# Performance work log

Measured on AMD Instinct MI355X. Metric: run time of the kernel, lower is better.

## Reference

```python
import jax, jax.numpy as jnp
import numpy as np

BS = 32  # block size
EPS = 1e-5

def _bn(h, g, b):
    # training-mode batchnorm over (N,H,W) of the gathered block batch
    mu = h.mean((0, 2, 3), keepdims=True)
    var = h.var((0, 2, 3), keepdims=True)
    return (h - mu) * jax.lax.rsqrt(var + EPS) * g.reshape(1, -1, 1, 1) + b.reshape(1, -1, 1, 1)

def setup_inputs() -> dict:
    key = jax.random.key(0)
    ks = jax.random.split(key, 12)
    B, Cin, H, W, Cout = 4, 128, 256, 256, 256
    Hb, Wb = H // BS, W // BS
    x = jax.random.normal(ks[0], (B, Cin, H, W), dtype=jnp.float32)
    rng = np.random.default_rng(0)
    flat = np.sort(rng.choice(B * Hb * Wb, size=128, replace=False)).astype(np.int32)
    bi = flat // (Hb * Wb)
    by = (flat % (Hb * Wb)) // Wb
    bx = flat % Wb
    block_idx = jnp.asarray(np.stack([bi, by, bx], axis=1), dtype=jnp.int32)  # [Nact,3]
    s1 = 1.0 / np.sqrt(Cin)
    s2 = 1.0 / np.sqrt(Cout * 9)
    return {
        "x": x,
        "w1": jax.random.normal(ks[1], (Cout, Cin), jnp.float32) * s1,
        "b1": jnp.zeros((Cout,), jnp.float32),
        "g1": jnp.ones((Cout,), jnp.float32),
        "be1": jnp.zeros((Cout,), jnp.float32),
        "w2": jax.random.normal(ks[2], (Cout, Cout, 3, 3), jnp.float32) * s2,
        "b2": jnp.zeros((Cout,), jnp.float32),
        "g2": jnp.ones((Cout,), jnp.float32),
        "be2": jnp.zeros((Cout,), jnp.float32),
        "wd": jax.random.normal(ks[3], (Cout, Cin), jnp.float32) * s1,
        "bd": jnp.zeros((Cout,), jnp.float32),
        "block_idx": block_idx,
    }

def reference(x, w1, b1, g1, be1, w2, b2, g2, be2, wd, bd, block_idx):
    B, Cin, H, W = x.shape
    Cout = w1.shape[0]
    Hb, Wb = H // BS, W // BS
    # --- sparse gather: [Nact, Cin, BS, BS] ---
    xb = x.reshape(B, Cin, Hb, BS, Wb, BS).transpose(0, 2, 4, 1, 3, 5)
    xb = xb.reshape(B * Hb * Wb, Cin, BS, BS)
    flat = block_idx[:, 0] * (Hb * Wb) + block_idx[:, 1] * Wb + block_idx[:, 2]
    dense = xb[flat]
    # --- dense conv stack on active blocks ---
    h = jnp.einsum('nchw,oc->nohw', dense, w1) + b1.reshape(1, -1, 1, 1)
    h = jax.nn.relu(_bn(h, g1, be1))  # relu is inplace in torch -> feeds conv2
    h = jax.lax.conv_general_dilated(h, w2, (1, 1), 'SAME',
                                     dimension_numbers=('NCHW', 'OIHW', 'NCHW'))
    h = h + b2.reshape(1, -1, 1, 1)
    dense_y = jax.nn.relu(_bn(h, g2, be2))
    # NOTE: original conv3/bn3 output is dead code (scatter uses dense_y); omitted.
    # --- dense base path (in_channels != out_channels -> downsample 1x1 conv) ---
    ybase = jnp.einsum('nchw,oc->nohw', x, wd) + bd.reshape(1, -1, 1, 1)
    # --- sparse scatter (overwrite, add=False) ---
    yb = ybase.reshape(B, Cout, Hb, BS, Wb, BS).transpose(0, 2, 4, 1, 3, 5)
    yb = yb.reshape(B * Hb * Wb, Cout, BS, BS)
    yb = yb.at[flat].set(dense_y)
    y = yb.reshape(B, Hb, Wb, Cout, BS, BS).transpose(0, 3, 1, 4, 2, 5)
    return y.reshape(B, Cout, H, W)
```

## Files before the change

kernel.cpp:

```cpp
#include <hip/hip_runtime.h>
#include <stdint.h>

#define CIN  128
#define COUT 256
#define HH   256
#define WW   256
#define BSZ  32
#define HB   8
#define WB   8
#define NBLK 256
#define P2   34
#define PIX2 1156

typedef __attribute__((ext_vector_type(8))) short bfx8;
typedef __attribute__((ext_vector_type(4))) float f32x4;

#define MFMA(a,b,c) __builtin_amdgcn_mfma_f32_16x16x32_bf16((a),(b),(c),0,0,0)

typedef const __attribute__((address_space(1))) unsigned int gu32;
typedef __attribute__((address_space(3))) unsigned int lu32;
#define GLOAD16(g, p) __builtin_amdgcn_global_load_lds((gu32*)(g), (lu32*)(p), 16, 0, 0)

static __device__ __forceinline__ float bf2f(unsigned short u){
  union { unsigned int i; float f; } v; v.i = ((unsigned int)u)<<16; return v.f;
}
static __device__ __forceinline__ unsigned short f2bf(float f){
  union { float f; unsigned int i; } v; v.f = f;
  unsigned int r = v.i + 0x7fffu + ((v.i>>16)&1u);
  return (unsigned short)(r>>16);
}

__global__ void k_prep(const float* __restrict__ w1, const float* __restrict__ wd,
                       const float* __restrict__ w2,
                       unsigned short* __restrict__ w1b, unsigned short* __restrict__ wdb,
                       unsigned short* __restrict__ w2t){
  int i = blockIdx.x*256 + threadIdx.x;
  if (i < COUT*CIN){ w1b[i] = f2bf(w1[i]); wdb[i] = f2bf(wd[i]); }
  if (i < COUT*COUT*9){
    int co = i/2304, r = i - co*2304;
    int ci = r/9,   tp = r - ci*9;
    w2t[((size_t)tp*COUT + co)*COUT + ci] = f2bf(w2[i]);
  }
}

__global__ void k_lists(const int* __restrict__ bidx, int nact,
                        int* __restrict__ flags, int* __restrict__ inact){
  int t = threadIdx.x;
  if (t < nact){
    int f = bidx[t*3]*(HB*WB) + bidx[t*3+1]*WB + bidx[t*3+2];
    flags[f] = 1;
  }
  __syncthreads();
  if (t == 0){
    int c = 0;
    for (int f = 0; f < NBLK; ++f) if (!flags[f]) inact[c++] = f;
  }
}

template<int MODE>
__global__ __launch_bounds__(256) void k_gemm1(
    const float* __restrict__ x, const unsigned short* __restrict__ wgt,
    const int* __restrict__ bidx, const int* __restrict__ inact,
    const float* __restrict__ bd, unsigned short* __restrict__ h1p,
    float* __restrict__ out, float* __restrict__ part){
  __shared__ unsigned short lds[2*5120];
  int rg = blockIdx.x, cot = blockIdx.y, z = blockIdx.z;
  int bi, by, bx;
  if (MODE == 0){ bi = bidx[z*3]; by = bidx[z*3+1]; bx = bidx[z*3+2]; }
  else { int fl = inact[z]; bi = fl>>6; by = (fl>>3)&7; bx = fl&7; }
  int t = threadIdx.x, l = t&63, wid = t>>6;
  int wc = wid>>1, wp = wid&1;
  int y0 = rg*4;
  int co_w = cot*128 + wc*64;

  const unsigned short* wb = wgt + (size_t)(co_w + (l&15))*CIN + ((l>>4)*8);
  bfx8 wfrag[4][4];
  #pragma unroll
  for (int kc = 0; kc < 4; ++kc)
    #pragma unroll
    for (int m = 0; m < 4; ++m)
      wfrag[kc][m] = *(const bfx8*)(wb + kc*32 + (size_t)m*16*CIN);

  const float* xb = x + (size_t)bi*CIN*HH*WW + (size_t)(by*BSZ + y0)*WW + bx*BSZ;
  float4 ra[2], rb_[2];
  auto ldreg = [&](int kc){
    #pragma unroll
    for (int j = 0; j < 2; ++j){
      int u = j*256 + t;
      int ci0 = (u>>5)*2 + kc*32;
      int p = (u&31)*4;
      const float* s = xb + (size_t)ci0*(HH*WW) + (p>>5)*WW + (p&31);
      ra[j]  = *(const float4*)s;
      rb_[j] = *(const float4*)(s + HH*WW);
    }
  };
  auto wrlds = [&](int buf){
    #pragma unroll
    for (int j = 0; j < 2; ++j){
      int u = j*256 + t;
      int ci0 = (u>>5)*2;
      int p = (u&31)*4;
      unsigned short* d = &lds[buf*5120 + ci0];
      *(ushort2*)&d[(p+0)*40] = make_ushort2(f2bf(ra[j].x), f2bf(rb_[j].x));
      *(ushort2*)&d[(p+1)*40] = make_ushort2(f2bf(ra[j].y), f2bf(rb_[j].y));
      *(ushort2*)&d[(p+2)*40] = make_ushort2(f2bf(ra[j].z), f2bf(rb_[j].z));
      *(ushort2*)&d[(p+3)*40] = make_ushort2(f2bf(ra[j].w), f2bf(rb_[j].w));
    }
  };

  f32x4 acc[4][4] = {};
  ldreg(0);
  for (int kc = 0; kc < 4; ++kc){
    wrlds(kc&1);
    if (kc < 3) ldreg(kc+1);
    __syncthreads();
    const unsigned short* lb = &lds[(kc&1)*5120];
    #pragma unroll
    for (int f = 0; f < 4; ++f){
      bfx8 b = *(const bfx8*)&lb[(wp*64 + f*16 + (l&15))*40 + (l>>4)*8];
      acc[0][f] = MFMA(wfrag[kc][0], b, acc[0][f]);
      acc[1][f] = MFMA(wfrag[kc][1], b, acc[1][f]);
      acc[2][f] = MFMA(wfrag[kc][2], b, acc[2][f]);
      acc[3][f] = MFMA(wfrag[kc][3], b, acc[3][f]);
    }
  }

  #pragma unroll
  for (int m = 0; m < 4; ++m){
    int co = co_w + m*16 + ((l>>4)<<2);
    #pragma unroll
    for (int f = 0; f < 4; ++f){
      int px = wp*64 + f*16 + (l&15);
      int ly = px>>5, lx = px&31;
      if (MODE == 0){
        *(ushort4*)&h1p[((size_t)z*PIX2 + (size_t)(y0+ly+1)*P2 + (lx+1))*COUT + co] =
          make_ushort4(f2bf(acc[m][f][0]), f2bf(acc[m][f][1]),
                       f2bf(acc[m][f][2]), f2bf(acc[m][f][3]));
      } else {
        int gy = by*BSZ + y0 + ly, gx = bx*BSZ + lx;
        #pragma unroll
        for (int j = 0; j < 4; ++j)
          out[(((size_t)bi*COUT + co + j)*HH + gy)*WW + gx] = acc[m][f][j] + bd[co+j];
      }
    }
  }

  if (MODE == 0){
    float s_[4][4], q_[4][4];
    #pragma unroll
    for (int m = 0; m < 4; ++m)
      #pragma unroll
      for (int j = 0; j < 4; ++j){
        float s = 0.f, q = 0.f;
        #pragma unroll
        for (int f = 0; f < 4; ++f){ float v = acc[m][f][j]; s += v; q += v*v; }
        s_[m][j] = s; q_[m][j] = q;
      }
    #pragma unroll
    for (int off = 1; off < 16; off <<= 1)
      #pragma unroll
      for (int m = 0; m < 4; ++m)
        #pragma unroll
        for (int j = 0; j < 4; ++j){
          s_[m][j] += __shfl_xor(s_[m][j], off);
          q_[m][j] += __shfl_xor(q_[m][j], off);
        }
    if ((l&15) == 0){
      int grp = z & 15;
      #pragma unroll
      for (int m = 0; m < 4; ++m)
        #pragma unroll
        for (int j = 0; j < 4; ++j){
          int co = co_w + m*16 + ((l>>4)<<2) + j;
          atomicAdd(&part[((size_t)grp*COUT + co)*2],   s_[m][j]);
          atomicAdd(&part[((size_t)grp*COUT + co)*2+1], q_[m][j]);
        }
    }
  }
}

__global__ void k_fin(const float* __restrict__ part, const float* __restrict__ g,
                      const float* __restrict__ be, float* __restrict__ st, float inv){
  int t = threadIdx.x;
  float s = 0.f, q = 0.f;
  #pragma unroll
  for (int gi = 0; gi < 16; ++gi){
    s += part[((size_t)gi*COUT + t)*2];
    q += part[((size_t)gi*COUT + t)*2+1];
  }
  float mu = s*inv, var = q*inv - mu*mu;
  float sc = g[t]*rsqrtf(var + 1e-5f);
  st[t] = sc; st[256+t] = be[t] - mu*sc;
}

__global__ void k_bn1(unsigned short* __restrict__ h1p, const float* __restrict__ st, int total){
  int t = threadIdx.x;
  int ci0 = (t&31)*8;
  float sc[8], tc[8];
  #pragma unroll
  for (int j = 0; j < 8; ++j){ sc[j] = st[ci0+j]; tc[j] = st[256+ci0+j]; }
  #pragma unroll
  for (int it = 0; it < 4; ++it){
    int gpix = blockIdx.x*32 + it*8 + (t>>5);
    if (gpix >= total) continue;
    int n = gpix/PIX2; int p = gpix - n*PIX2;
    int row = p/P2, col = p - row*P2;
    unsigned short* addr = h1p + (size_t)gpix*COUT + ci0;
    if (row >= 1 && row <= 32 && col >= 1 && col <= 32){
      bfx8 v = *(bfx8*)addr;
      unsigned short o[8];
      #pragma unroll
      for (int j = 0; j < 8; ++j){
        float f = bf2f(((unsigned short*)&v)[j]);
        o[j] = f2bf(fmaxf(f*sc[j] + tc[j], 0.f));
      }
      *(bfx8*)addr = *(bfx8*)o;
    } else {
      bfx8 z = {};
      *(bfx8*)addr = z;
    }
  }
}

__global__ __launch_bounds__(512, 4) void k_conv2(
    const unsigned short* __restrict__ h1p, const unsigned short* __restrict__ w2t,
    const int* __restrict__ bidx, float* __restrict__ out, float* __restrict__ part){
  __shared__ unsigned short lds[24576];
  int bxid = blockIdx.x, n = blockIdx.y;
  int h = bxid & 1, q = bxid >> 1;
  int bi = bidx[n*3], by = bidx[n*3+1], bx = bidx[n*3+2];
  int t = threadIdx.x, l = t&63, wid = t>>6;
  int wm = wid>>1, wn = wid&1;
  int y0 = q*8;

  int offA[4], offB[2];
  #pragma unroll
  for (int j = 0; j < 4; ++j){
    int i = j*512 + t;
    int row = i>>3, sl_ = i&7;
    offA[j] = row*COUT + (sl_ ^ (row&7))*8;
  }
  #pragma unroll
  for (int j = 0; j < 2; ++j){
    int i = j*512 + t;
    int row = i>>3, sl_ = i&7;
    offB[j] = ((row>>5)*P2 + (row&31))*COUT + (sl_ ^ (row&7))*8;
  }
  const unsigned short* h1q = h1p + ((size_t)n*PIX2 + (size_t)(y0 + h*4)*P2)*COUT;

  int lr = l&15, lh = l>>4;
  f32x4 acc[4][4] = {};

  for (int s = 0; s < 36; ++s){
    int tp = s>>2, cc = s&3;
    int dy = tp/3, dx = tp - dy*3;
    const unsigned short* wsrc = w2t + (size_t)tp*COUT*COUT + cc*64;
    const unsigned short* psrc = h1q + (size_t)(dy*P2 + dx)*COUT + cc*64;
    __syncthreads();
    #pragma unroll
    for (int j = 0; j < 4; ++j)
      GLOAD16(wsrc + offA[j], &lds[(j*512 + t)*8]);
    #pragma unroll
    for (int j = 0; j < 2; ++j)
      GLOAD16(psrc + offB[j], &lds[16384 + (j*512 + t)*8]);
    __syncthreads();
    #pragma unroll
    for (int kk = 0; kk < 2; ++kk){
      bfx8 af[4], bfr[4];
      #pragma unroll
      for (int m = 0; m < 4; ++m)
        af[m] = *(const bfx8*)&lds[(wm*64 + m*16 + lr)*64 + ((kk*4 + lh) ^ (lr&7))*8];
      #pragma unroll
      for (int nn = 0; nn < 4; ++nn)
        bfr[nn] = *(const bfx8*)&lds[16384 + (wn*64 + nn*16 + lr)*64 + ((kk*4 + lh) ^ (lr&7))*8];
      #pragma unroll
      for (int m = 0; m < 4; ++m)
        #pragma unroll
        for (int nn = 0; nn < 4; ++nn)
          acc[m][nn] = MFMA(af[m], bfr[nn], acc[m][nn]);
    }
  }

  #pragma unroll
  for (int m = 0; m < 4; ++m){
    int co = wm*64 + m*16 + lh*4;
    #pragma unroll
    for (int nn = 0; nn < 4; ++nn){
      int px = h*128 + wn*64 + nn*16 + lr;
      int gy = by*BSZ + y0 + (px>>5), gx = bx*BSZ + (px&31);
      #pragma unroll
      for (int j = 0; j < 4; ++j)
        out[(((size_t)bi*COUT + co + j)*HH + gy)*WW + gx] = acc[m][nn][j];
    }
  }

  #pragma unroll
  for (int m = 0; m < 4; ++m){
    #pragma unroll
    for (int j = 0; j < 4; ++j){
      float s = 0.f, qq = 0.f;
      #pragma unroll
      for (int nn = 0; nn < 4; ++nn){ float v = acc[m][nn][j]; s += v; qq += v*v; }
      #pragma unroll
      for (int off = 1; off < 16; off <<= 1){
        s  += __shfl_xor(s,  off);
        qq += __shfl_xor(qq, off);
      }
      if (lr == 0){
        int co = wm*64 + m*16 + lh*4 + j;
        atomicAdd(&part[((size_t)(n&15)*COUT + co)*2],   s);
        atomicAdd(&part[((size_t)(n&15)*COUT + co)*2+1], qq);
      }
    }
  }
}

__global__ void k_bn2(float* __restrict__ out, const int* __restrict__ bidx,
                      const float* __restrict__ st){
  int cq = blockIdx.x, n = blockIdx.y, t = threadIdx.x;
  int bi = bidx[n*3], by = bidx[n*3+1], bx = bidx[n*3+2];
  int px0 = t*4; int ly = px0>>5, lx = px0&31;
  float* base = out + (size_t)bi*COUT*HH*WW + (size_t)(by*BSZ+ly)*WW + bx*BSZ + lx;
  for (int c = 0; c < 64; ++c){
    int co = cq*64 + c;
    float sc = st[co], tc = st[256+co];
    float4* p = (float4*)(base + (size_t)co*HH*WW);
    float4 v = *p;
    v.x = fmaxf(v.x*sc+tc, 0.f); v.y = fmaxf(v.y*sc+tc, 0.f);
    v.z = fmaxf(v.z*sc+tc, 0.f); v.w = fmaxf(v.w*sc+tc, 0.f);
    *p = v;
  }
}

extern "C" void kernel_launch(void* const* d_in, const int* in_sizes, int n_in,
                              void* d_out, int out_size, void* d_ws, size_t ws_size,
                              hipStream_t stream){
  const float* x   = (const float*)d_in[0];
  const float* w1  = (const float*)d_in[1];
  const float* g1  = (const float*)d_in[3];
  const float* be1 = (const float*)d_in[4];
  const float* w2  = (const float*)d_in[5];
  const float* g2  = (const float*)d_in[7];
  const float* be2 = (const float*)d_in[8];
  const float* wd  = (const float*)d_in[9];
  const float* bd  = (const float*)d_in[10];
  const int* bidx  = (const int*)d_in[11];
  float* out = (float*)d_out;
  const int nact = in_sizes[11]/3;
  const int ninact = NBLK - nact;

  char* wsp = (char*)d_ws;
  size_t off = 0;
  auto carve = [&](size_t bytes)->char*{
    char* p = wsp + off; off += (bytes + 255) & ~(size_t)255; return p;
  };
  unsigned short* h1p = (unsigned short*)carve((size_t)nact*PIX2*COUT*2 + 4096);
  unsigned short* w1b = (unsigned short*)carve((size_t)COUT*CIN*2);
  unsigned short* wdb = (unsigned short*)carve((size_t)COUT*CIN*2);
  unsigned short* w2t = (unsigned short*)carve((size_t)9*COUT*COUT*2);
  float* s1t1  = (float*)carve(512*4);
  float* s2t2  = (float*)carve(512*4);
  float* part1 = (float*)carve((size_t)16*COUT*2*4);
  float* part2 = (float*)carve((size_t)16*COUT*2*4);
  int* flags   = (int*)carve(NBLK*4);
  int* inact   = (int*)carve(NBLK*4);

  hipMemsetAsync(flags, 0, NBLK*4, stream);
  hipMemsetAsync(part1, 0, (size_t)16*COUT*2*4, stream);
  hipMemsetAsync(part2, 0, (size_t)16*COUT*2*4, stream);
  k_lists<<<1, 256, 0, stream>>>(bidx, nact, flags, inact);
  k_prep<<<2304, 256, 0, stream>>>(w1, wd, w2, w1b, wdb, w2t);
  k_gemm1<0><<<dim3(8, 2, nact), 256, 0, stream>>>(x, w1b, bidx, inact, bd, h1p, out, part1);
  k_fin<<<1, 256, 0, stream>>>(part1, g1, be1, s1t1, 1.0f/((float)nact*1024.0f));
  {
    int total = nact*PIX2;
    k_bn1<<<(total + 31)/32, 256, 0, stream>>>(h1p, s1t1, total);
  }
  k_conv2<<<dim3(8, nact), 512, 0, stream>>>(h1p, w2t, bidx, out, part2);
  k_fin<<<1, 256, 0, stream>>>(part2, g2, be2, s2t2, 1.0f/((float)nact*1024.0f));
  if (ninact > 0)
    k_gemm1<1><<<dim3(8, 2, ninact), 256, 0, stream>>>(x, wdb, bidx, inact, bd, h1p, out, part1);
  k_bn2<<<dim3(4, nact), 256, 0, stream>>>(out, bidx, s2t2);
}
```

Before: 431.5 us.

## Restructure conv2: double-buffer activation tiles, load weights directly from global

The conv2 implicit-GEMM kernel now uses 256-thread blocks, each covering 128 output channels by 128 pixels, with a 16xN grid. Activation tiles are double-buffered in LDS so the next tap's global->LDS load overlaps the current MFMA work, leaving one barrier per step. Weight fragments are read straight from global memory, relying on cache, instead of being staged through LDS. This halves LDS use and barrier count, but each wave now issues uncoalesced-ish global weight loads inside the inner loop.

New measurement: 632.9 us. 46.7% more time.

```diff
diff --git a/kernel.cpp b/kernel.cpp
--- a/kernel.cpp
+++ b/kernel.cpp
@@ -222,71 +222,74 @@
   }
 }
 
-__global__ __launch_bounds__(512, 4) void k_conv2(
+__global__ __launch_bounds__(256, 3) void k_conv2(
     const unsigned short* __restrict__ h1p, const unsigned short* __restrict__ w2t,
     const int* __restrict__ bidx, float* __restrict__ out, float* __restrict__ part){
-  __shared__ unsigned short lds[24576];
-  int bxid = blockIdx.x, n = blockIdx.y;
-  int h = bxid & 1, q = bxid >> 1;
+  __shared__ unsigned short lds[2*8192];
+  int xx = blockIdx.x, n = blockIdx.y;
+  int coh = xx & 1, ph = xx >> 1;
   int bi = bidx[n*3], by = bidx[n*3+1], bx = bidx[n*3+2];
   int t = threadIdx.x, l = t&63, wid = t>>6;
   int wm = wid>>1, wn = wid&1;
-  int y0 = q*8;
-
-  int offA[4], offB[2];
+  int y0 = ph*4;
+  int co_w = coh*128 + wm*64;
+  int lr = l&15, lh = l>>4;
+
+  int offB[4];
   #pragma unroll
   for (int j = 0; j < 4; ++j){
-    int i = j*512 + t;
+    int i = j*256 + t;
     int row = i>>3, sl_ = i&7;
-    offA[j] = row*COUT + (sl_ ^ (row&7))*8;
-  }
-  #pragma unroll
-  for (int j = 0; j < 2; ++j){
-    int i = j*512 + t;
-    int row = i>>3, sl_ = i&7;
-    offB[j] = ((row>>5)*P2 + (row&31))*COUT + (sl_ ^ (row&7))*8;
-  }
-  const unsigned short* h1q = h1p + ((size_t)n*PIX2 + (size_t)(y0 + h*4)*P2)*COUT;
-
-  int lr = l&15, lh = l>>4;
-  f32x4 acc[4][4] = {};
-
-  for (int s = 0; s < 36; ++s){
+    offB[j] = ((row>>5)*P2 + (row&31))*COUT + ((sl_ ^ (row&7))*8);
+  }
+  const unsigned short* h1q = h1p + ((size_t)n*PIX2 + (size_t)y0*P2)*COUT;
+
+  auto stageB = [&](int buf, int s){
     int tp = s>>2, cc = s&3;
     int dy = tp/3, dx = tp - dy*3;
-    const unsigned short* wsrc = w2t + (size_t)tp*COUT*COUT + cc*64;
     const unsigned short* psrc = h1q + (size_t)(dy*P2 + dx)*COUT + cc*64;
-    __syncthreads();
     #pragma unroll
     for (int j = 0; j < 4; ++j)
-      GLOAD16(wsrc + offA[j], &lds[(j*512 + t)*8]);
-    #pragma unroll
-    for (int j = 0; j < 2; ++j)
-      GLOAD16(psrc + offB[j], &lds[16384 + (j*512 + t)*8]);
-    __syncthreads();
+      GLOAD16(psrc + offB[j], &lds[buf*8192 + (j*256 + t)*8]);
+  };
+
+  const unsigned short* aW = w2t + (size_t)(co_w + lr)*COUT + lh*8;
+
+  f32x4 acc[4][4] = {};
+  stageB(0, 0);
+  __syncthreads();
+  for (int s = 0; s < 36; ++s){
+    int cur = s&1;
+    if (s < 35) stageB(cur^1, s+1);
+    int tp = s>>2, cc = s&3;
+    const unsigned short* aS = aW + (size_t)tp*COUT*COUT + cc*64;
+    const unsigned short* Bb = &lds[cur*8192];
     #pragma unroll
     for (int kk = 0; kk < 2; ++kk){
       bfx8 af[4], bfr[4];
       #pragma unroll
       for (int m = 0; m < 4; ++m)
-        af[m] = *(const bfx8*)&lds[(wm*64 + m*16 + lr)*64 + ((kk*4 + lh) ^ (lr&7))*8];
-      #pragma unroll
-      for (int nn = 0; nn < 4; ++nn)
-        bfr[nn] = *(const bfx8*)&lds[16384 + (wn*64 + nn*16 + lr)*64 + ((kk*4 + lh) ^ (lr&7))*8];
+        af[m] = *(const bfx8*)(aS + (size_t)(m*16)*COUT + kk*32);
+      #pragma unroll
+      for (int nn = 0; nn < 4; ++nn){
+        int r = wn*64 + nn*16 + lr;
+        bfr[nn] = *(const bfx8*)&Bb[r*64 + (((kk*4 + lh) ^ (r&7))*8)];
+      }
       #pragma unroll
       for (int m = 0; m < 4; ++m)
         #pragma unroll
         for (int nn = 0; nn < 4; ++nn)
           acc[m][nn] = MFMA(af[m], bfr[nn], acc[m][nn]);
     }
+    __syncthreads();
   }
 
   #pragma unroll
   for (int m = 0; m < 4; ++m){
-    int co = wm*64 + m*16 + lh*4;
+    int co = co_w + m*16 + lh*4;
     #pragma unroll
     for (int nn = 0; nn < 4; ++nn){
-      int px = h*128 + wn*64 + nn*16 + lr;
+      int px = wn*64 + nn*16 + lr;
       int gy = by*BSZ + y0 + (px>>5), gx = bx*BSZ + (px&31);
       #pragma unroll
       for (int j = 0; j < 4; ++j)
@@ -307,7 +310,7 @@
         qq += __shfl_xor(qq, off);
       }
       if (lr == 0){
-        int co = wm*64 + m*16 + lh*4 + j;
+        int co = co_w + m*16 + lh*4 + j;
         atomicAdd(&part[((size_t)(n&15)*COUT + co)*2],   s);
         atomicAdd(&part[((size_t)(n&15)*COUT + co)*2+1], qq);
       }
@@ -376,7 +379,7 @@
     int total = nact*PIX2;
     k_bn1<<<(total + 31)/32, 256, 0, stream>>>(h1p, s1t1, total);
   }
-  k_conv2<<<dim3(8, nact), 512, 0, stream>>>(h1p, w2t, bidx, out, part2);
+  k_conv2<<<dim3(16, nact), 256, 0, stream>>>(h1p, w2t, bidx, out, part2);
   k_fin<<<1, 256, 0, stream>>>(part2, g2, be2, s2t2, 1.0f/((float)nact*1024.0f));
   if (ninact > 0)
     k_gemm1<1><<<dim3(8, 2, ninact), 256, 0, stream>>>(x, wdb, bidx, inact, bd, h1p, out, part1);
```

## Restructure conv2 into 256x256 tiles with 32x32 MFMA and double-buffered LDS

Applied to the files above, without the earlier changes.

The conv2 implicit GEMM moves from 512-thread blocks computing 256x128 tiles with 16x16x32 MFMA to 256-thread blocks computing 256 channels by 256 pixels with 32x32x16 MFMA. Global-to-LDS loads are double-buffered, with an explicit vmcnt wait so the next stage's loads overlap the current stage's compute. Block IDs are swizzled across XCDs. The larger per-thread accumulator (256 floats) and 128KB of LDS limit occupancy to one block per CU. The grid also shrinks to nact*4 blocks, about 512, which is under two waves across the device's CUs.

New measurement: 478.2 us. 1.11x slower.

```diff
diff --git a/kernel.cpp b/kernel.cpp
--- a/kernel.cpp
+++ b/kernel.cpp
@@ -14,8 +14,10 @@
 
 typedef __attribute__((ext_vector_type(8))) short bfx8;
 typedef __attribute__((ext_vector_type(4))) float f32x4;
-
-#define MFMA(a,b,c) __builtin_amdgcn_mfma_f32_16x16x32_bf16((a),(b),(c),0,0,0)
+typedef __attribute__((ext_vector_type(16))) float f32x16;
+
+#define MFMA(a,b,c)   __builtin_amdgcn_mfma_f32_16x16x32_bf16((a),(b),(c),0,0,0)
+#define MFMA32(a,b,c) __builtin_amdgcn_mfma_f32_32x32x16_bf16((a),(b),(c),0,0,0)
 
 typedef const __attribute__((address_space(1))) unsigned int gu32;
 typedef __attribute__((address_space(3))) unsigned int lu32;
@@ -222,92 +224,106 @@
   }
 }
 
-__global__ __launch_bounds__(512, 4) void k_conv2(
+__global__ __launch_bounds__(256, 1) void k_conv2(
     const unsigned short* __restrict__ h1p, const unsigned short* __restrict__ w2t,
     const int* __restrict__ bidx, float* __restrict__ out, float* __restrict__ part){
-  __shared__ unsigned short lds[24576];
-  int bxid = blockIdx.x, n = blockIdx.y;
-  int h = bxid & 1, q = bxid >> 1;
+  __shared__ unsigned short lds[65536];
+  int bid = blockIdx.x;
+  int swz = (bid & 7)*64 + (bid >> 3);
+  int n = swz >> 2, q = swz & 3;
   int bi = bidx[n*3], by = bidx[n*3+1], bx = bidx[n*3+2];
   int t = threadIdx.x, l = t&63, wid = t>>6;
   int wm = wid>>1, wn = wid&1;
   int y0 = q*8;
 
-  int offA[4], offB[2];
-  #pragma unroll
-  for (int j = 0; j < 4; ++j){
-    int i = j*512 + t;
+  int offA[8], offB[8];
+  #pragma unroll
+  for (int j = 0; j < 8; ++j){
+    int i = j*256 + t;
     int row = i>>3, sl_ = i&7;
     offA[j] = row*COUT + (sl_ ^ (row&7))*8;
-  }
-  #pragma unroll
-  for (int j = 0; j < 2; ++j){
-    int i = j*512 + t;
-    int row = i>>3, sl_ = i&7;
     offB[j] = ((row>>5)*P2 + (row&31))*COUT + (sl_ ^ (row&7))*8;
   }
-  const unsigned short* h1q = h1p + ((size_t)n*PIX2 + (size_t)(y0 + h*4)*P2)*COUT;
-
-  int lr = l&15, lh = l>>4;
-  f32x4 acc[4][4] = {};
-
-  for (int s = 0; s < 36; ++s){
+  const unsigned short* h1q = h1p + ((size_t)n*PIX2 + (size_t)y0*P2)*COUT;
+
+  auto stage = [&](int buf, int s){
     int tp = s>>2, cc = s&3;
     int dy = tp/3, dx = tp - dy*3;
     const unsigned short* wsrc = w2t + (size_t)tp*COUT*COUT + cc*64;
     const unsigned short* psrc = h1q + (size_t)(dy*P2 + dx)*COUT + cc*64;
-    __syncthreads();
-    #pragma unroll
-    for (int j = 0; j < 4; ++j)
-      GLOAD16(wsrc + offA[j], &lds[(j*512 + t)*8]);
-    #pragma unroll
-    for (int j = 0; j < 2; ++j)
-      GLOAD16(psrc + offB[j], &lds[16384 + (j*512 + t)*8]);
-    __syncthreads();
-    #pragma unroll
-    for (int kk = 0; kk < 2; ++kk){
-      bfx8 af[4], bfr[4];
+    #pragma unroll
+    for (int j = 0; j < 8; ++j)
+      GLOAD16(wsrc + offA[j], &lds[buf*32768 + (j*256 + t)*8]);
+    #pragma unroll
+    for (int j = 0; j < 8; ++j)
+      GLOAD16(psrc + offB[j], &lds[buf*32768 + 16384 + (j*256 + t)*8]);
+  };
+
+  int l31 = l&31, lh = l>>5, l7 = l&7;
+  f32x16 acc[4][4] = {};
+
+  stage(0, 0);
+  for (int s = 0; s < 36; ++s){
+    int cur = s&1;
+    if (s < 35){
+      stage(cur^1, s+1);
+      asm volatile("s_waitcnt vmcnt(16)" ::: "memory");
+    } else {
+      asm volatile("s_waitcnt vmcnt(0)" ::: "memory");
+    }
+    __builtin_amdgcn_s_barrier();
+    const unsigned short* Ab = &lds[cur*32768];
+    const unsigned short* Bb = &lds[cur*32768 + 16384];
+    #pragma unroll
+    for (int kk = 0; kk < 4; ++kk){
+      int oct = (kk*2 + lh) ^ l7;
+      bfx8 a[4], b[4];
       #pragma unroll
       for (int m = 0; m < 4; ++m)
-        af[m] = *(const bfx8*)&lds[(wm*64 + m*16 + lr)*64 + ((kk*4 + lh) ^ (lr&7))*8];
+        a[m] = *(const bfx8*)&Ab[(wm*128 + m*32 + l31)*64 + oct*8];
       #pragma unroll
       for (int nn = 0; nn < 4; ++nn)
-        bfr[nn] = *(const bfx8*)&lds[16384 + (wn*64 + nn*16 + lr)*64 + ((kk*4 + lh) ^ (lr&7))*8];
+        b[nn] = *(const bfx8*)&Bb[(wn*128 + nn*32 + l31)*64 + oct*8];
       #pragma unroll
       for (int m = 0; m < 4; ++m)
         #pragma unroll
         for (int nn = 0; nn < 4; ++nn)
-          acc[m][nn] = MFMA(af[m], bfr[nn], acc[m][nn]);
-    }
+          acc[m][nn] = MFMA32(a[m], b[nn], acc[m][nn]);
+    }
+    __builtin_amdgcn_s_barrier();
   }
 
   #pragma unroll
   for (int m = 0; m < 4; ++m){
-    int co = wm*64 + m*16 + lh*4;
+    int cm = wm*128 + m*32 + 4*lh;
     #pragma unroll
     for (int nn = 0; nn < 4; ++nn){
-      int px = h*128 + wn*64 + nn*16 + lr;
+      int px = wn*128 + nn*32 + l31;
       int gy = by*BSZ + y0 + (px>>5), gx = bx*BSZ + (px&31);
-      #pragma unroll
-      for (int j = 0; j < 4; ++j)
-        out[(((size_t)bi*COUT + co + j)*HH + gy)*WW + gx] = acc[m][nn][j];
+      float* ob = out + ((size_t)bi*COUT*HH + (size_t)gy)*WW + gx;
+      #pragma unroll
+      for (int r = 0; r < 16; ++r){
+        int co = cm + (r&3) + 8*(r>>2);
+        ob[(size_t)co*HH*WW] = acc[m][nn][r];
+      }
     }
   }
 
   #pragma unroll
   for (int m = 0; m < 4; ++m){
-    #pragma unroll
-    for (int j = 0; j < 4; ++j){
+    int cm = wm*128 + m*32 + 4*lh;
+    #pragma unroll
+    for (int r = 0; r < 16; ++r){
       float s = 0.f, qq = 0.f;
       #pragma unroll
-      for (int nn = 0; nn < 4; ++nn){ float v = acc[m][nn][j]; s += v; qq += v*v; }
-      #pragma unroll
-      for (int off = 1; off < 16; off <<= 1){
+      for (int nn = 0; nn < 4; ++nn){ float v = acc[m][nn][r]; s += v; qq += v*v; }
+      #pragma unroll
+      for (int off = 1; off < 32; off <<= 1){
         s  += __shfl_xor(s,  off);
         qq += __shfl_xor(qq, off);
       }
-      if (lr == 0){
-        int co = wm*64 + m*16 + lh*4 + j;
+      if (l31 == 0){
+        int co = cm + (r&3) + 8*(r>>2);
         atomicAdd(&part[((size_t)(n&15)*COUT + co)*2],   s);
         atomicAdd(&part[((size_t)(n&15)*COUT + co)*2+1], qq);
       }
@@ -376,7 +392,7 @@
     int total = nact*PIX2;
     k_bn1<<<(total + 31)/32, 256, 0, stream>>>(h1p, s1t1, total);
   }
-  k_conv2<<<dim3(8, nact), 512, 0, stream>>>(h1p, w2t, bidx, out, part2);
+  k_conv2<<<dim3(nact*4), 256, 0, stream>>>(h1p, w2t, bidx, out, part2);
   k_fin<<<1, 256, 0, stream>>>(part2, g2, be2, s2t2, 1.0f/((float)nact*1024.0f));
   if (ninact > 0)
     k_gemm1<1><<<dim3(8, 2, ninact), 256, 0, stream>>>(x, wdb, bidx, inact, bd, h1p, out, part1);
```

## Remap grid for XCD-local L2 reuse and use nontemporal output stores

Applied to the files above, without the earlier changes.

Flattens the gemm1 and conv2 grids and remaps block ids so blocks dispatched to the same XCD work on neighbouring data, aiming for better L2 locality. Output writes in gemm1 and conv2, and the read-modify-write in bn2, use nontemporal loads and stores to avoid polluting cache with streaming data. conv2 launch bounds raise the min-blocks hint to 6, which may force fewer registers and spills. The conv2 remap hardcodes 128 active blocks.

Measured after the change: 1.099 ms. +154.7%, slower.

```diff
diff --git a/kernel.cpp b/kernel.cpp
--- a/kernel.cpp
+++ b/kernel.cpp
@@ -62,9 +62,14 @@
     const float* __restrict__ x, const unsigned short* __restrict__ wgt,
     const int* __restrict__ bidx, const int* __restrict__ inact,
     const float* __restrict__ bd, unsigned short* __restrict__ h1p,
-    float* __restrict__ out, float* __restrict__ part){
+    float* __restrict__ out, float* __restrict__ part, int nb){
   __shared__ unsigned short lds[2*5120];
-  int rg = blockIdx.x, cot = blockIdx.y, z = blockIdx.z;
+  int chunk = nb*2;
+  int bid = blockIdx.x;
+  int id = (bid & 7)*chunk + (bid >> 3);
+  int rg = id / chunk;
+  int rem = id - rg*chunk;
+  int z = rem >> 1, cot = rem & 1;
   int bi, by, bx;
   if (MODE == 0){ bi = bidx[z*3]; by = bidx[z*3+1]; bx = bidx[z*3+2]; }
   else { int fl = inact[z]; bi = fl>>6; by = (fl>>3)&7; bx = fl&7; }
@@ -140,7 +145,8 @@
         int gy = by*BSZ + y0 + ly, gx = bx*BSZ + lx;
         #pragma unroll
         for (int j = 0; j < 4; ++j)
-          out[(((size_t)bi*COUT + co + j)*HH + gy)*WW + gx] = acc[m][f][j] + bd[co+j];
+          __builtin_nontemporal_store(acc[m][f][j] + bd[co+j],
+              &out[(((size_t)bi*COUT + co + j)*HH + gy)*WW + gx]);
       }
     }
   }
@@ -222,11 +228,13 @@
   }
 }
 
-__global__ __launch_bounds__(512, 4) void k_conv2(
+__global__ __launch_bounds__(512, 6) void k_conv2(
     const unsigned short* __restrict__ h1p, const unsigned short* __restrict__ w2t,
     const int* __restrict__ bidx, float* __restrict__ out, float* __restrict__ part){
   __shared__ unsigned short lds[24576];
-  int bxid = blockIdx.x, n = blockIdx.y;
+  int bid = blockIdx.x;
+  int id = (bid & 7)*128 + (bid >> 3);
+  int n = id >> 3, bxid = id & 7;
   int h = bxid & 1, q = bxid >> 1;
   int bi = bidx[n*3], by = bidx[n*3+1], bx = bidx[n*3+2];
   int t = threadIdx.x, l = t&63, wid = t>>6;
@@ -290,7 +298,8 @@
       int gy = by*BSZ + y0 + (px>>5), gx = bx*BSZ + (px&31);
       #pragma unroll
       for (int j = 0; j < 4; ++j)
-        out[(((size_t)bi*COUT + co + j)*HH + gy)*WW + gx] = acc[m][nn][j];
+        __builtin_nontemporal_store(acc[m][nn][j],
+            &out[(((size_t)bi*COUT + co + j)*HH + gy)*WW + gx]);
     }
   }
 
@@ -324,11 +333,12 @@
   for (int c = 0; c < 64; ++c){
     int co = cq*64 + c;
     float sc = st[co], tc = st[256+co];
-    float4* p = (float4*)(base + (size_t)co*HH*WW);
-    float4 v = *p;
-    v.x = fmaxf(v.x*sc+tc, 0.f); v.y = fmaxf(v.y*sc+tc, 0.f);
-    v.z = fmaxf(v.z*sc+tc, 0.f); v.w = fmaxf(v.w*sc+tc, 0.f);
-    *p = v;
+    f32x4* p = (f32x4*)(base + (size_t)co*HH*WW);
+    f32x4 v = __builtin_nontemporal_load(p);
+    f32x4 r;
+    r.x = fmaxf(v.x*sc+tc, 0.f); r.y = fmaxf(v.y*sc+tc, 0.f);
+    r.z = fmaxf(v.z*sc+tc, 0.f); r.w = fmaxf(v.w*sc+tc, 0.f);
+    __builtin_nontemporal_store(r, p);
   }
 }
 
@@ -370,15 +380,15 @@
   hipMemsetAsync(part2, 0, (size_t)16*COUT*2*4, stream);
   k_lists<<<1, 256, 0, stream>>>(bidx, nact, flags, inact);
   k_prep<<<2304, 256, 0, stream>>>(w1, wd, w2, w1b, wdb, w2t);
-  k_gemm1<0><<<dim3(8, 2, nact), 256, 0, stream>>>(x, w1b, bidx, inact, bd, h1p, out, part1);
+  k_gemm1<0><<<dim3(16*nact), 256, 0, stream>>>(x, w1b, bidx, inact, bd, h1p, out, part1, nact);
   k_fin<<<1, 256, 0, stream>>>(part1, g1, be1, s1t1, 1.0f/((float)nact*1024.0f));
   {
     int total = nact*PIX2;
     k_bn1<<<(total + 31)/32, 256, 0, stream>>>(h1p, s1t1, total);
   }
-  k_conv2<<<dim3(8, nact), 512, 0, stream>>>(h1p, w2t, bidx, out, part2);
+  k_conv2<<<dim3(nact*8), 512, 0, stream>>>(h1p, w2t, bidx, out, part2);
   k_fin<<<1, 256, 0, stream>>>(part2, g2, be2, s2t2, 1.0f/((float)nact*1024.0f));
   if (ninact > 0)
-    k_gemm1<1><<<dim3(8, 2, ninact), 256, 0, stream>>>(x, wdb, bidx, inact, bd, h1p, out, part1);
+    k_gemm1<1><<<dim3(16*ninact), 256, 0, stream>>>(x, wdb, bidx, inact, bd, h1p, out, part1, ninact);
   k_bn2<<<dim3(4, nact), 256, 0, stream>>>(out, bidx, s2t2);
 }
```
